# Kernel optimization log

Hardware: AMD Instinct MI355X
Metric: run time of the kernel (lower is better)

The kernel has to match this reference:

```python
import jax, jax.numpy as jnp
import numpy as np

B, H, S, DK = 1, 16, 4096, 64
SQRT_DK = float(DK) ** 0.5


def setup_inputs() -> dict:
    key = jax.random.key(0)
    kq, kk, kv = jax.random.split(key, 3)
    q = jax.random.normal(kq, (B, H, S, DK), dtype=jnp.float32)
    k = jax.random.normal(kk, (B, H, S, DK), dtype=jnp.float32)
    v = jax.random.normal(kv, (B, H, S, DK), dtype=jnp.float32)
    # causal mask: 1 where attention allowed, 0 where masked
    mask = jnp.tril(jnp.ones((S, S), dtype=jnp.int32))[None, None, :, :]
    return {"q": q, "k": k, "v": v, "mask": mask}


def reference(q, k, v, mask):
    # score = q @ k^T / sqrt(d_k)  -> [B, H, S, S]
    score = jnp.einsum("bhqd,bhkd->bhqk", q, k) / SQRT_DK
    # masked_fill(mask == 0, -inf)
    score = jnp.where(mask == 0, -jnp.inf, score)
    attn = jax.nn.softmax(score, axis=-1)
    # dropout with p=0.0 is identity
    return jnp.einsum("bhqk,bhkd->bhqd", attn, v)
```

## Files before the change

kernel.cpp:

```cpp
#include <hip/hip_runtime.h>

#define NH 16
#define SEQ 4096
#define DK 64
#define LSTR 72

typedef __fp16   fp16x2 __attribute__((ext_vector_type(2)));
typedef _Float16 f16x2 __attribute__((ext_vector_type(2)));
typedef _Float16 f16x4 __attribute__((ext_vector_type(4)));
typedef _Float16 f16x8 __attribute__((ext_vector_type(8)));
typedef float    f32x4 __attribute__((ext_vector_type(4)));

__device__ __forceinline__ f16x4 pk4(float a, float b, float c, float d) {
    f16x2 lo = __builtin_bit_cast(f16x2, (fp16x2)__builtin_amdgcn_cvt_pkrtz(a, b));
    f16x2 hi = __builtin_bit_cast(f16x2, (fp16x2)__builtin_amdgcn_cvt_pkrtz(c, d));
    f16x4 r; r[0]=lo[0]; r[1]=lo[1]; r[2]=hi[0]; r[3]=hi[1];
    return r;
}
__device__ __forceinline__ f16x8 pk8(float4 a, float4 b) {
    f16x4 lo = pk4(a.x, a.y, a.z, a.w);
    f16x4 hi = pk4(b.x, b.y, b.z, b.w);
    f16x8 r;
    r[0]=lo[0]; r[1]=lo[1]; r[2]=lo[2]; r[3]=lo[3];
    r[4]=hi[0]; r[5]=hi[1]; r[6]=hi[2]; r[7]=hi[3];
    return r;
}
__device__ __forceinline__ f16x4 lo4(f16x8 x){return __builtin_shufflevector(x,x,0,1,2,3);}
__device__ __forceinline__ f16x4 hi4(f16x8 x){return __builtin_shufflevector(x,x,4,5,6,7);}

__global__ __launch_bounds__(256) void sdpa_flash_v7(
    const float* __restrict__ q, const float* __restrict__ k,
    const float* __restrict__ v, float* __restrict__ out)
{
    __shared__ _Float16 Ks[2][64 * LSTR];
    __shared__ _Float16 Vt[2][64 * LSTR];

    const int t    = threadIdx.x;
    const int wave = t >> 6;
    const int lane = t & 63;
    const int ln   = lane & 15;
    const int quad = lane >> 4;

    const int h  = blockIdx.x & (NH - 1);
    const int qt = 63 - (blockIdx.x >> 4);
    const int q0 = qt * 64;
    const int qw = q0 + wave * 16;

    const float SC = 0.125f * 1.44269504088896f;

    const float* qrow = q + ((size_t)h * SEQ + qw + ln) * DK;
    f16x8 qf[2];
#pragma unroll
    for (int kk = 0; kk < 2; ++kk) {
        float4 a = *(const float4*)(qrow + kk * 32 + quad * 8);
        float4 b = *(const float4*)(qrow + kk * 32 + quad * 8 + 4);
        qf[kk] = pk8(a, b);
    }

    f32x4 O[4];
#pragma unroll
    for (int i = 0; i < 4; ++i) O[i] = (f32x4){0.f, 0.f, 0.f, 0.f};
    float l = 0.f;

    const float4* kh4 = (const float4*)(k + (size_t)h * SEQ * DK);
    const float*  vhp = v + (size_t)h * SEQ * DK;
    const int vd = lane;

    float4 kpre[4];
    float  vpre[4][4];
#pragma unroll
    for (int i = 0; i < 4; ++i) {
        kpre[i] = kh4[i * 256 + t];
        const float* vp = vhp + (size_t)(4 * (i * 4 + wave)) * DK + vd;
#pragma unroll
        for (int j = 0; j < 4; ++j) vpre[i][j] = vp[j * DK];
    }

    int buf = 0;
    for (int k0 = 0; k0 <= q0; k0 += 64) {
#pragma unroll
        for (int i = 0; i < 4; ++i) {
            const int idx = i * 256 + t;
            const int key = idx >> 4, c4 = idx & 15;
            *(f16x4*)&Ks[buf][key * LSTR + c4 * 4] =
                pk4(kpre[i].x, kpre[i].y, kpre[i].z, kpre[i].w);
            const int m = i * 4 + wave;
            const int c = (m & 3) * 16 + (m >> 2) * 4;
            *(f16x4*)&Vt[buf][vd * LSTR + c] =
                pk4(vpre[i][0], vpre[i][1], vpre[i][2], vpre[i][3]);
        }
        __syncthreads();

        if (k0 < q0) {
            const int kn = k0 + 64;
#pragma unroll
            for (int i = 0; i < 4; ++i) {
                kpre[i] = kh4[kn * 16 + i * 256 + t];
                const float* vp = vhp + (size_t)(kn + 4 * (i * 4 + wave)) * DK + vd;
#pragma unroll
                for (int j = 0; j < 4; ++j) vpre[i][j] = vp[j * DK];
            }
        }

        const bool diag = (k0 + 63 > qw);
        f16x4 pf[4];
#pragma unroll
        for (int ksub = 0; ksub < 4; ++ksub) {
            const _Float16* kr = &Ks[buf][(ksub * 16 + ln) * LSTR + quad * 8];
            f16x8 a0 = *(const f16x8*)kr;
            f16x8 a1 = *(const f16x8*)(kr + 32);
            f32x4 acc = (f32x4){0.f, 0.f, 0.f, 0.f};
            acc = __builtin_amdgcn_mfma_f32_16x16x32_f16(a0, qf[0], acc, 0, 0, 0);
            acc = __builtin_amdgcn_mfma_f32_16x16x32_f16(a1, qf[1], acc, 0, 0, 0);
            if (diag) {
                const int keyb = k0 + ksub * 16 + quad * 4;
#pragma unroll
                for (int r = 0; r < 4; ++r)
                    if (keyb + r > qw + ln) acc[r] = -1e30f;
            }
            float p0 = __builtin_amdgcn_exp2f(fmaf(acc[0], SC, -12.f));
            float p1 = __builtin_amdgcn_exp2f(fmaf(acc[1], SC, -12.f));
            float p2 = __builtin_amdgcn_exp2f(fmaf(acc[2], SC, -12.f));
            float p3 = __builtin_amdgcn_exp2f(fmaf(acc[3], SC, -12.f));
            l += (p0 + p1) + (p2 + p3);
            pf[ksub] = pk4(p0, p1, p2, p3);
        }
#pragma unroll
        for (int dsub = 0; dsub < 4; ++dsub) {
            const _Float16* vr = &Vt[buf][(dsub * 16 + ln) * LSTR + quad * 16];
            f16x8 v01 = *(const f16x8*)vr;
            f16x8 v23 = *(const f16x8*)(vr + 8);
            O[dsub] = __builtin_amdgcn_mfma_f32_16x16x16f16(lo4(v01), pf[0], O[dsub], 0, 0, 0);
            O[dsub] = __builtin_amdgcn_mfma_f32_16x16x16f16(hi4(v01), pf[1], O[dsub], 0, 0, 0);
            O[dsub] = __builtin_amdgcn_mfma_f32_16x16x16f16(lo4(v23), pf[2], O[dsub], 0, 0, 0);
            O[dsub] = __builtin_amdgcn_mfma_f32_16x16x16f16(hi4(v23), pf[3], O[dsub], 0, 0, 0);
        }
        buf ^= 1;
    }

    l += __shfl_xor(l, 16);
    l += __shfl_xor(l, 32);
    const float inv = 1.f / l;
    float* op = out + ((size_t)h * SEQ + qw + ln) * DK + quad * 4;
#pragma unroll
    for (int dsub = 0; dsub < 4; ++dsub) {
        float4 r;
        r.x = O[dsub][0] * inv; r.y = O[dsub][1] * inv;
        r.z = O[dsub][2] * inv; r.w = O[dsub][3] * inv;
        *(float4*)(op + dsub * 16) = r;
    }
}

extern "C" void kernel_launch(void* const* d_in, const int* in_sizes, int n_in,
                              void* d_out, int out_size, void* d_ws, size_t ws_size,
                              hipStream_t stream) {
    const float* q = (const float*)d_in[0];
    const float* k = (const float*)d_in[1];
    const float* v = (const float*)d_in[2];
    float* out = (float*)d_out;

    dim3 grid(NH * 64);
    dim3 block(256);
    sdpa_flash_v7<<<grid, block, 0, stream>>>(q, k, v, out);
}
```

Before: 199.4 us.

## Split long causal query tiles across key chunks with atomic-coordinated reduction

Long causal query tiles are split into several key-range chunks, each handled by its own block, so work per block is more even and the grid is larger. Partial unnormalized outputs and row sums go to workspace slots in fp16. The last-arriving block, tracked with atomic counters, waits for the other chunks, adds their results and writes the normalized output. This adds a workspace memset, extra global traffic, spin-waiting and some fp16 precision loss on the partials.

```diff
diff --git a/kernel.cpp b/kernel.cpp
--- a/kernel.cpp
+++ b/kernel.cpp
@@ -4,6 +4,8 @@
 #define SEQ 4096
 #define DK 64
 #define LSTR 72
+#define SLOT_BYTES 8448
+#define HEAD_SLOTS 90
 
 typedef __fp16   fp16x2 __attribute__((ext_vector_type(2)));
 typedef _Float16 f16x2 __attribute__((ext_vector_type(2)));
@@ -28,12 +30,20 @@
 __device__ __forceinline__ f16x4 lo4(f16x8 x){return __builtin_shufflevector(x,x,0,1,2,3);}
 __device__ __forceinline__ f16x4 hi4(f16x8 x){return __builtin_shufflevector(x,x,4,5,6,7);}
 
-__global__ __launch_bounds__(256) void sdpa_flash_v7(
+__device__ __forceinline__ int slot_prefix(int qt) {
+    return (qt <= 33) ? (qt - 17)
+         : (qt <= 50) ? (17 + 2 * (qt - 34))
+                      : (51 + 3 * (qt - 51));
+}
+
+__global__ __launch_bounds__(256, 8) void sdpa_flash_v8(
     const float* __restrict__ q, const float* __restrict__ k,
-    const float* __restrict__ v, float* __restrict__ out)
+    const float* __restrict__ v, float* __restrict__ out,
+    char* __restrict__ ws)
 {
     __shared__ _Float16 Ks[2][64 * LSTR];
     __shared__ _Float16 Vt[2][64 * LSTR];
+    __shared__ int s_a;
 
     const int t    = threadIdx.x;
     const int wave = t >> 6;
@@ -41,10 +51,19 @@
     const int ln   = lane & 15;
     const int quad = lane >> 4;
 
-    const int h  = blockIdx.x & (NH - 1);
-    const int qt = 63 - (blockIdx.x >> 4);
-    const int q0 = qt * 64;
-    const int qw = q0 + wave * 16;
+    const int h = blockIdx.x & (NH - 1);
+    int s = blockIdx.x >> 4;
+    int qt = 0, c = 0;
+    for (int q2 = 63, acc = 0; q2 >= 0; --q2) {
+        const int n = (q2 + 17) / 17;
+        if (s < acc + n) { qt = q2; c = s - acc; break; }
+        acc += n;
+    }
+    const int T   = qt + 1;
+    const int nch = (qt + 17) / 17;
+    const int kb0 = (c * T) / nch, kb1 = ((c + 1) * T) / nch;
+
+    const int qw = qt * 64 + wave * 16;
 
     const float SC = 0.125f * 1.44269504088896f;
 
@@ -70,14 +89,15 @@
     float  vpre[4][4];
 #pragma unroll
     for (int i = 0; i < 4; ++i) {
-        kpre[i] = kh4[i * 256 + t];
-        const float* vp = vhp + (size_t)(4 * (i * 4 + wave)) * DK + vd;
+        kpre[i] = kh4[kb0 * 1024 + i * 256 + t];
+        const float* vp = vhp + (size_t)(kb0 * 64 + 4 * (i * 4 + wave)) * DK + vd;
 #pragma unroll
         for (int j = 0; j < 4; ++j) vpre[i][j] = vp[j * DK];
     }
 
     int buf = 0;
-    for (int k0 = 0; k0 <= q0; k0 += 64) {
+    for (int kb = kb0; kb < kb1; ++kb) {
+        const int k0 = kb * 64;
 #pragma unroll
         for (int i = 0; i < 4; ++i) {
             const int idx = i * 256 + t;
@@ -85,14 +105,14 @@
             *(f16x4*)&Ks[buf][key * LSTR + c4 * 4] =
                 pk4(kpre[i].x, kpre[i].y, kpre[i].z, kpre[i].w);
             const int m = i * 4 + wave;
-            const int c = (m & 3) * 16 + (m >> 2) * 4;
-            *(f16x4*)&Vt[buf][vd * LSTR + c] =
+            const int cc = (m & 3) * 16 + (m >> 2) * 4;
+            *(f16x4*)&Vt[buf][vd * LSTR + cc] =
                 pk4(vpre[i][0], vpre[i][1], vpre[i][2], vpre[i][3]);
         }
         __syncthreads();
 
-        if (k0 < q0) {
-            const int kn = k0 + 64;
+        if (kb + 1 < kb1) {
+            const int kn = (kb + 1) * 64;
 #pragma unroll
             for (int i = 0; i < 4; ++i) {
                 kpre[i] = kh4[kn * 16 + i * 256 + t];
@@ -140,14 +160,72 @@
 
     l += __shfl_xor(l, 16);
     l += __shfl_xor(l, 32);
-    const float inv = 1.f / l;
-    float* op = out + ((size_t)h * SEQ + qw + ln) * DK + quad * 4;
-#pragma unroll
-    for (int dsub = 0; dsub < 4; ++dsub) {
-        float4 r;
-        r.x = O[dsub][0] * inv; r.y = O[dsub][1] * inv;
-        r.z = O[dsub][2] * inv; r.w = O[dsub][3] * inv;
-        *(float4*)(op + dsub * 16) = r;
+
+    if (nch == 1) {
+        const float inv = 1.f / l;
+        float* op = out + ((size_t)h * SEQ + qw + ln) * DK + quad * 4;
+#pragma unroll
+        for (int dsub = 0; dsub < 4; ++dsub) {
+            float4 r;
+            r.x = O[dsub][0] * inv; r.y = O[dsub][1] * inv;
+            r.z = O[dsub][2] * inv; r.w = O[dsub][3] * inv;
+            *(float4*)(op + dsub * 16) = r;
+        }
+        return;
+    }
+
+    int* pre  = (int*)ws + (h * 64 + qt);
+    int* done = (int*)ws + 1024 + (h * 64 + qt);
+    char* slots = ws + 8192;
+    const int gbase = h * HEAD_SLOTS + slot_prefix(qt);
+    const int row = wave * 16 + ln;
+
+    if (t == 0) s_a = atomicAdd(pre, 1);
+    __syncthreads();
+    const int a = s_a;
+
+    if (a < nch - 1) {
+        char* slot = slots + (size_t)(gbase + a) * SLOT_BYTES;
+        _Float16* Op = (_Float16*)slot;
+        float*    Lp = (float*)(slot + 8192);
+#pragma unroll
+        for (int dsub = 0; dsub < 4; ++dsub)
+            *(f16x4*)&Op[row * 64 + dsub * 16 + quad * 4] =
+                pk4(O[dsub][0], O[dsub][1], O[dsub][2], O[dsub][3]);
+        if (quad == 0) Lp[row] = l;
+        __threadfence();
+        __syncthreads();
+        if (t == 0) atomicAdd(done, 1);
+    } else {
+        if (t == 0) {
+            while (__hip_atomic_load(done, __ATOMIC_ACQUIRE,
+                                     __HIP_MEMORY_SCOPE_AGENT) < nch - 1)
+                __builtin_amdgcn_s_sleep(8);
+        }
+        __syncthreads();
+        __threadfence();
+#pragma unroll 1
+        for (int a2 = 0; a2 < nch - 1; ++a2) {
+            char* slot = slots + (size_t)(gbase + a2) * SLOT_BYTES;
+            const _Float16* Op = (const _Float16*)slot;
+            const float*    Lp = (const float*)(slot + 8192);
+            l += Lp[row];
+#pragma unroll
+            for (int dsub = 0; dsub < 4; ++dsub) {
+                f16x4 o2 = *(const f16x4*)&Op[row * 64 + dsub * 16 + quad * 4];
+#pragma unroll
+                for (int r = 0; r < 4; ++r) O[dsub][r] += (float)o2[r];
+            }
+        }
+        const float inv = 1.f / l;
+        float* op = out + ((size_t)h * SEQ + qw + ln) * DK + quad * 4;
+#pragma unroll
+        for (int dsub = 0; dsub < 4; ++dsub) {
+            float4 r;
+            r.x = O[dsub][0] * inv; r.y = O[dsub][1] * inv;
+            r.z = O[dsub][2] * inv; r.w = O[dsub][3] * inv;
+            *(float4*)(op + dsub * 16) = r;
+        }
     }
 }
 
@@ -159,7 +237,9 @@
     const float* v = (const float*)d_in[2];
     float* out = (float*)d_out;
 
-    dim3 grid(NH * 64);
+    hipMemsetAsync(d_ws, 0, 8192, stream);
+
+    dim3 grid(NH * 154);
     dim3 block(256);
-    sdpa_flash_v7<<<grid, block, 0, stream>>>(q, k, v, out);
-}
+    sdpa_flash_v8<<<grid, block, 0, stream>>>(q, k, v, out, (char*)d_ws);
+}
```

New measurement: 488.6 us. 145% more time.
